# Kernel optimization log

Measured on AMD Instinct MI355X. Metric: run time of the kernel, lower is better.

Reference implementation:

```python
import jax, jax.numpy as jnp
import numpy as np

K = 16  # kNN neighbors (global k in the original source)
# channel progression of the 6 DynamicEdgeConv layers
DIMS = [3, 32, 128, 256, 64, 32, 16]


def _knn_idx(x, k):
    # x: [B, N, D] -> indices of k nearest neighbors (incl. self), [B, N, k]
    sq = jnp.sum(x * x, axis=-1)                                   # [B, N]
    d = sq[:, :, None] + sq[:, None, :] - 2.0 * jnp.einsum('bnd,bmd->bnm', x, x)
    _, idx = jax.lax.top_k(-d, k)                                  # smallest distances
    return idx


def _edge_conv(x, W1, b1, W2, b2, k):
    # DynamicEdgeConv with mean aggregation: message = MLP([x_i, x_j - x_i])
    idx = _knn_idx(x, k)                                           # [B, N, k]
    xj = jax.vmap(lambda xb, ib: xb[ib])(x, idx)                   # [B, N, k, D]
    xi = jnp.broadcast_to(x[:, :, None, :], xj.shape)
    e = jnp.concatenate([xi, xj - xi], axis=-1)                    # [B, N, k, 2D]
    h = jax.nn.relu(e @ W1 + b1)
    h = jax.nn.relu(h @ W2 + b2)
    return jnp.mean(h, axis=2)                                     # [B, N, d_out]


def setup_inputs() -> dict:
    key = jax.random.key(0)
    ks = jax.random.split(key, 32)
    inp = {'x': jax.random.normal(ks[0], (8, 2048, 3), dtype=jnp.float32)}
    for l in range(6):
        din, dout = DIMS[l], DIMS[l + 1]
        s1 = 1.0 / np.sqrt(2 * din)
        s2 = 1.0 / np.sqrt(2 * dout)
        inp[f'W1_{l}'] = jax.random.normal(ks[1 + 4 * l], (2 * din, 2 * dout), dtype=jnp.float32) * s1
        inp[f'b1_{l}'] = jnp.zeros((2 * dout,), dtype=jnp.float32)
        inp[f'W2_{l}'] = jax.random.normal(ks[2 + 4 * l], (2 * dout, dout), dtype=jnp.float32) * s2
        inp[f'b2_{l}'] = jnp.zeros((dout,), dtype=jnp.float32)
    inp['Wf'] = jax.random.normal(ks[30], (16, 2), dtype=jnp.float32) * 0.25
    inp['bf'] = jnp.zeros((2,), dtype=jnp.float32)
    return inp


def reference(x, W1_0, b1_0, W2_0, b2_0, W1_1, b1_1, W2_1, b2_1,
              W1_2, b1_2, W2_2, b2_2, W1_3, b1_3, W2_3, b2_3,
              W1_4, b1_4, W2_4, b2_4, W1_5, b1_5, W2_5, b2_5, Wf, bf):
    params = [(W1_0, b1_0, W2_0, b2_0), (W1_1, b1_1, W2_1, b2_1),
              (W1_2, b1_2, W2_2, b2_2), (W1_3, b1_3, W2_3, b2_3),
              (W1_4, b1_4, W2_4, b2_4), (W1_5, b1_5, W2_5, b2_5)]
    for (W1, b1, W2, b2) in params:
        x = _edge_conv(x, W1, b1, W2, b2, K)
        x = jax.nn.relu(x)  # extra ReLU from forward (dropout is eval-mode identity)
    pooled = jnp.mean(x, axis=1)        # global_mean_pool over nodes -> [B, 16]
    return pooled @ Wf + bf             # [B, 2]
```

## Files before the change

### kernel.cpp

```cpp
#include <hip/hip_runtime.h>
#include <math.h>

#define NPTS 2048
#define NB 8
#define BN 16384
#define KNN 16

typedef _Float16 half4 __attribute__((ext_vector_type(4)));
typedef _Float16 half8 __attribute__((ext_vector_type(8)));
typedef float floatx16 __attribute__((ext_vector_type(16)));

__global__ __launch_bounds__(256) void sqprep_kernel(const float* __restrict__ X,
                                                     float* __restrict__ SQ,
                                                     const float* __restrict__ W1,
                                                     const float* __restrict__ b1,
                                                     float* __restrict__ Wcat,
                                                     float* __restrict__ bcat,
                                                     int din, int d2,
                                                     const float* __restrict__ W2,
                                                     _Float16* __restrict__ W2H,
                                                     _Float16* __restrict__ W2L,
                                                     int dout, int pb) {
    const int bid = blockIdx.x;
    if (bid < BN / 256) {
        int g = bid * 256 + threadIdx.x;
        const float* row = X + (size_t)g * din;
        float s = 0.f;
        for (int d = 0; d < din; ++d) s = fmaf(row[d], row[d], s);
        SQ[g] = s;
    } else if (bid < BN / 256 + pb) {
        int n4 = 2 * d2;
        int total = din * n4;
        int i = (bid - BN / 256) * 256 + threadIdx.x;
        if (i < total) {
            int d = i / n4, c = i - d * n4;
            float v;
            if (c < d2) v = W1[d * d2 + c] - W1[(din + d) * d2 + c];
            else        v = W1[(din + d) * d2 + (c - d2)];
            Wcat[i] = v;
        }
        if (i < n4) bcat[i] = (i < d2) ? b1[i] : 0.f;
    } else {
        int i = (bid - BN / 256 - pb) * 256 + threadIdx.x;
        if (i < d2 * dout) {
            int k = i / dout, c = i - k * dout;
            float wv = W2[i];
            _Float16 hv = (_Float16)wv;
            float rv = wv - (float)hv;
            W2H[(size_t)c * d2 + k] = hv;
            W2L[(size_t)c * d2 + k] = (_Float16)rv;
        }
    }
}

template <int DIN>
__global__ __launch_bounds__(256) void gram_kernel(const float* __restrict__ X,
                                                   const float* __restrict__ SQ,
                                                   float* __restrict__ DT) {
    __shared__ float As[32][132];
    __shared__ float Bs[32][132];
    const int t = threadIdx.x;
    const int tx = t & 15, ty = t >> 4;
    int bid = blockIdx.x;
    int bi = 0;
    while (bid >= 16 - bi) { bid -= 16 - bi; ++bi; }
    const int bj = bi + bid;
    const int i0 = bi * 128;
    const int j0 = bj * 128;
    const int z = blockIdx.z;
    const float* Xb = X + (size_t)z * NPTS * DIN;
    const float* SQb = SQ + (size_t)z * NPTS;
    float* DTb = DT + (size_t)z * NPTS * NPTS;

    const int e = t & 127;

    float acc[8][8];
    #pragma unroll
    for (int i = 0; i < 8; ++i)
        #pragma unroll
        for (int j = 0; j < 8; ++j) acc[i][j] = 0.f;

    if constexpr (DIN % 32 == 0) {
        const int rh = (t >> 7) * 16;
        const float* Ar = Xb + (size_t)(i0 + e) * DIN;
        const float* Br = Xb + (size_t)(j0 + e) * DIN;
        for (int k0 = 0; k0 < DIN; k0 += 32) {
            #pragma unroll
            for (int h = 0; h < 4; ++h) {
                float4 a = *(const float4*)(Ar + k0 + rh + h * 4);
                float4 b = *(const float4*)(Br + k0 + rh + h * 4);
                As[rh + h * 4 + 0][e] = a.x; As[rh + h * 4 + 1][e] = a.y;
                As[rh + h * 4 + 2][e] = a.z; As[rh + h * 4 + 3][e] = a.w;
                Bs[rh + h * 4 + 0][e] = b.x; Bs[rh + h * 4 + 1][e] = b.y;
                Bs[rh + h * 4 + 2][e] = b.z; Bs[rh + h * 4 + 3][e] = b.w;
            }
            __syncthreads();
            #pragma unroll
            for (int r = 0; r < 32; ++r) {
                float4 a0 = *(const float4*)&As[r][ty * 4];
                float4 a1 = *(const float4*)&As[r][64 + ty * 4];
                float4 b0 = *(const float4*)&Bs[r][tx * 4];
                float4 b1 = *(const float4*)&Bs[r][64 + tx * 4];
                float av[8] = {a0.x, a0.y, a0.z, a0.w, a1.x, a1.y, a1.z, a1.w};
                float bv[8] = {b0.x, b0.y, b0.z, b0.w, b1.x, b1.y, b1.z, b1.w};
                #pragma unroll
                for (int i = 0; i < 8; ++i)
                    #pragma unroll
                    for (int j = 0; j < 8; ++j)
                        acc[i][j] = fmaf(av[i], bv[j], acc[i][j]);
            }
            __syncthreads();
        }
    } else {
        const int rh = (t >> 7) * 8;
        #pragma unroll
        for (int i = 0; i < 8; ++i) {
            int k = rh + i;
            As[rh + i][e] = (k < DIN) ? Xb[(size_t)(i0 + e) * DIN + k] : 0.f;
            Bs[rh + i][e] = (k < DIN) ? Xb[(size_t)(j0 + e) * DIN + k] : 0.f;
        }
        __syncthreads();
        #pragma unroll
        for (int r = 0; r < 16; ++r) {
            float4 a0 = *(const float4*)&As[r][ty * 4];
            float4 a1 = *(const float4*)&As[r][64 + ty * 4];
            float4 b0 = *(const float4*)&Bs[r][tx * 4];
            float4 b1 = *(const float4*)&Bs[r][64 + tx * 4];
            float av[8] = {a0.x, a0.y, a0.z, a0.w, a1.x, a1.y, a1.z, a1.w};
            float bv[8] = {b0.x, b0.y, b0.z, b0.w, b1.x, b1.y, b1.z, b1.w};
            #pragma unroll
            for (int i = 0; i < 8; ++i)
                #pragma unroll
                for (int j = 0; j < 8; ++j)
                    acc[i][j] = fmaf(av[i], bv[j], acc[i][j]);
        }
        __syncthreads();
    }

    float sqi[8], sqj[8];
    #pragma unroll
    for (int i = 0; i < 8; ++i) {
        int ro = (i < 4) ? (ty * 4 + i) : (64 + ty * 4 + (i - 4));
        sqi[i] = SQb[i0 + ro];
    }
    #pragma unroll
    for (int j = 0; j < 8; ++j) {
        int co = (j < 4) ? (tx * 4 + j) : (64 + tx * 4 + (j - 4));
        sqj[j] = SQb[j0 + co];
    }
    #pragma unroll
    for (int i = 0; i < 8; ++i) {
        int ro = (i < 4) ? (ty * 4 + i) : (64 + ty * 4 + (i - 4));
        float* out = DTb + (size_t)(i0 + ro) * NPTS + j0;
        float4 o0, o1;
        o0.x = (sqi[i] + sqj[0]) - 2.f * acc[i][0];
        o0.y = (sqi[i] + sqj[1]) - 2.f * acc[i][1];
        o0.z = (sqi[i] + sqj[2]) - 2.f * acc[i][2];
        o0.w = (sqi[i] + sqj[3]) - 2.f * acc[i][3];
        o1.x = (sqi[i] + sqj[4]) - 2.f * acc[i][4];
        o1.y = (sqi[i] + sqj[5]) - 2.f * acc[i][5];
        o1.z = (sqi[i] + sqj[6]) - 2.f * acc[i][6];
        o1.w = (sqi[i] + sqj[7]) - 2.f * acc[i][7];
        *(float4*)(out + tx * 4) = o0;
        *(float4*)(out + 64 + tx * 4) = o1;
    }
    if (bi != bj) {
        #pragma unroll
        for (int j = 0; j < 8; ++j) {
            int co = (j < 4) ? (tx * 4 + j) : (64 + tx * 4 + (j - 4));
            float* out = DTb + (size_t)(j0 + co) * NPTS + i0;
            float4 o0, o1;
            o0.x = (sqi[0] + sqj[j]) - 2.f * acc[0][j];
            o0.y = (sqi[1] + sqj[j]) - 2.f * acc[1][j];
            o0.z = (sqi[2] + sqj[j]) - 2.f * acc[2][j];
            o0.w = (sqi[3] + sqj[j]) - 2.f * acc[3][j];
            o1.x = (sqi[4] + sqj[j]) - 2.f * acc[4][j];
            o1.y = (sqi[5] + sqj[j]) - 2.f * acc[5][j];
            o1.z = (sqi[6] + sqj[j]) - 2.f * acc[6][j];
            o1.w = (sqi[7] + sqj[j]) - 2.f * acc[7][j];
            *(float4*)(out + ty * 4) = o0;
            *(float4*)(out + 64 + ty * 4) = o1;
        }
    }
}

__global__ __launch_bounds__(256) void knn_select_kernel(const float* __restrict__ DT,
                                                         int* __restrict__ IDX, int qoff) {
    const int t = threadIdx.x;
    const int w = t >> 6, lane = t & 63;
    const int q = blockIdx.x * 4 + w;
    const float* dq = DT + (size_t)q * NPTS;
    const int l4 = lane << 2;

    float vals[32];
    #pragma unroll
    for (int s = 0; s < 8; ++s) {
        float4 v = *(const float4*)(dq + s * 256 + l4);
        vals[s * 4 + 0] = v.x; vals[s * 4 + 1] = v.y;
        vals[s * 4 + 2] = v.z; vals[s * 4 + 3] = v.w;
    }
    unsigned rm = 0;
    float best = INFINITY; int bslot = 32;
    #pragma unroll
    for (int sl = 0; sl < 32; ++sl)
        if (vals[sl] < best) { best = vals[sl]; bslot = sl; }

    for (int rep = 0; rep < KNN; ++rep) {
        int bj = (bslot < 32) ? ((bslot >> 2) * 256 + l4 + (bslot & 3)) : NPTS;
        float gb = best; int gj = bj;
        #pragma unroll
        for (int off = 1; off < 64; off <<= 1) {
            float ov = __shfl_xor(gb, off);
            int oj = __shfl_xor(gj, off);
            if (ov < gb || (ov == gb && oj < gj)) { gb = ov; gj = oj; }
        }
        if (lane == 0) IDX[(size_t)(qoff + q) * KNN + rep] = gj;
        if (((gj >> 2) & 63) == lane) {
            int slot = ((gj >> 8) << 2) | (gj & 3);
            rm |= (1u << slot);
            best = INFINITY; bslot = 32;
            #pragma unroll
            for (int sl = 0; sl < 32; ++sl)
                if (!(rm & (1u << sl)) && vals[sl] < best) { best = vals[sl]; bslot = sl; }
        }
    }
}

template <int KK, int NN>
__global__ __launch_bounds__(256) void gemm_big_kernel(const float* __restrict__ A,
                                                       const float* __restrict__ B,
                                                       const float* __restrict__ bias,
                                                       float* __restrict__ C) {
    __shared__ float As[32][132];
    __shared__ float Bs[32][132];
    const int t = threadIdx.x;
    const int tx = t & 15, ty = t >> 4;
    const int m0 = blockIdx.x * 128;
    const int c0 = blockIdx.y * 128;

    float acc[8][8];
    #pragma unroll
    for (int i = 0; i < 8; ++i)
        #pragma unroll
        for (int j = 0; j < 8; ++j) acc[i][j] = 0.f;

    const int e = t & 127;
    const int rh = (t >> 7) * 16;
    const float* Ar = A + (size_t)(m0 + e) * KK + rh;
    const int br = t & 31;
    const int bc = (t >> 5) * 16;
    const float* Wbase = B + (size_t)br * NN + c0 + bc;

    for (int k0 = 0; k0 < KK; k0 += 32) {
        #pragma unroll
        for (int h = 0; h < 4; ++h) {
            float4 a = *(const float4*)(Ar + k0 + h * 4);
            As[rh + h * 4 + 0][e] = a.x; As[rh + h * 4 + 1][e] = a.y;
            As[rh + h * 4 + 2][e] = a.z; As[rh + h * 4 + 3][e] = a.w;
            *(float4*)&Bs[br][bc + h * 4] = *(const float4*)(Wbase + (size_t)k0 * NN + h * 4);
        }
        __syncthreads();
        #pragma unroll
        for (int r = 0; r < 32; ++r) {
            float4 a0 = *(const float4*)&As[r][ty * 4];
            float4 a1 = *(const float4*)&As[r][64 + ty * 4];
            float4 b0 = *(const float4*)&Bs[r][tx * 4];
            float4 b1 = *(const float4*)&Bs[r][64 + tx * 4];
            float av[8] = {a0.x, a0.y, a0.z, a0.w, a1.x, a1.y, a1.z, a1.w};
            float bv[8] = {b0.x, b0.y, b0.z, b0.w, b1.x, b1.y, b1.z, b1.w};
            #pragma unroll
            for (int i = 0; i < 8; ++i)
                #pragma unroll
                for (int j = 0; j < 8; ++j)
                    acc[i][j] = fmaf(av[i], bv[j], acc[i][j]);
        }
        __syncthreads();
    }

    float bvv[8];
    #pragma unroll
    for (int j = 0; j < 8; ++j) {
        int co = (j < 4) ? (tx * 4 + j) : (64 + tx * 4 + (j - 4));
        bvv[j] = bias[c0 + co];
    }
    #pragma unroll
    for (int i = 0; i < 8; ++i) {
        int ro = (i < 4) ? (ty * 4 + i) : (64 + ty * 4 + (i - 4));
        float* out = C + (size_t)(m0 + ro) * NN + c0;
        float4 o0, o1;
        o0.x = acc[i][0] + bvv[0]; o0.y = acc[i][1] + bvv[1];
        o0.z = acc[i][2] + bvv[2]; o0.w = acc[i][3] + bvv[3];
        o1.x = acc[i][4] + bvv[4]; o1.y = acc[i][5] + bvv[5];
        o1.z = acc[i][6] + bvv[6]; o1.w = acc[i][7] + bvv[7];
        *(float4*)(out + tx * 4) = o0;
        *(float4*)(out + 64 + tx * 4) = o1;
    }
}

template <int KK, int NN>
__global__ __launch_bounds__(256) void gemm_pq_kernel(const float* __restrict__ A,
                                                      const float* __restrict__ B,
                                                      const float* __restrict__ bias,
                                                      float* __restrict__ C) {
    __shared__ float As[16][68];
    __shared__ float Bs[16][64];
    const int t = threadIdx.x;
    const int tx = t & 15, ty = t >> 4;
    const int m0 = blockIdx.x * 64;
    const int c0 = blockIdx.y * 64;
    float acc[4][4];
    #pragma unroll
    for (int i = 0; i < 4; ++i)
        #pragma unroll
        for (int j = 0; j < 4; ++j) acc[i][j] = 0.f;

    constexpr int KCH = (KK + 15) / 16;
    for (int kc = 0; kc < KCH; ++kc) {
        const int k0 = kc * 16;
        {
            int m = t & 63;
            int r4 = (t >> 6) * 4;
            if constexpr (KK % 16 == 0) {
                float4 v = *(const float4*)(A + (size_t)(m0 + m) * KK + k0 + r4);
                As[r4 + 0][m] = v.x; As[r4 + 1][m] = v.y;
                As[r4 + 2][m] = v.z; As[r4 + 3][m] = v.w;
            } else {
                #pragma unroll
                for (int i = 0; i < 4; ++i) {
                    int r = r4 + i;
                    As[r][m] = (k0 + r < KK) ? A[(size_t)(m0 + m) * KK + k0 + r] : 0.f;
                }
            }
        }
        {
            int r = t >> 4;
            int c = (t & 15) * 4;
            float4 v = make_float4(0.f, 0.f, 0.f, 0.f);
            if (k0 + r < KK) v = *(const float4*)(B + (size_t)(k0 + r) * NN + c0 + c);
            *(float4*)&Bs[r][c] = v;
        }
        __syncthreads();
        #pragma unroll
        for (int r = 0; r < 16; ++r) {
            float4 a4 = *(const float4*)&As[r][ty * 4];
            float4 b4 = *(const float4*)&Bs[r][tx * 4];
            float av[4] = {a4.x, a4.y, a4.z, a4.w};
            float bv[4] = {b4.x, b4.y, b4.z, b4.w};
            #pragma unroll
            for (int i = 0; i < 4; ++i)
                #pragma unroll
                for (int j = 0; j < 4; ++j)
                    acc[i][j] = fmaf(av[i], bv[j], acc[i][j]);
        }
        __syncthreads();
    }
    float4 bv4 = *(const float4*)(bias + c0 + tx * 4);
    float bv[4] = {bv4.x, bv4.y, bv4.z, bv4.w};
    #pragma unroll
    for (int i = 0; i < 4; ++i) {
        float4 o;
        o.x = acc[i][0] + bv[0];
        o.y = acc[i][1] + bv[1];
        o.z = acc[i][2] + bv[2];
        o.w = acc[i][3] + bv[3];
        *(float4*)(C + (size_t)(m0 + ty * 4 + i) * NN + c0 + tx * 4) = o;
    }
}

template <int D2, int DOUT>
__global__ __launch_bounds__(256) void edge_kernel(const float* __restrict__ PQ,
                                                   const int* __restrict__ IDX,
                                                   const float* __restrict__ W2,
                                                   const float* __restrict__ b2,
                                                   float* __restrict__ Xn) {
    constexpr int N4 = 2 * D2;
    __shared__ float As[16][68];
    __shared__ float Bs[16][64];
    __shared__ int gjs[64];
    const int t = threadIdx.x;
    const int tx = t & 15, ty = t >> 4;
    const int nb = blockIdx.x * 4;
    const int c0 = blockIdx.y * 64;

    if (t < 64) {
        int node = nb + (t >> 4);
        int bstart = (node / NPTS) * NPTS;
        gjs[t] = bstart + IDX[(size_t)node * KNN + (t & 15)];
    }
    __syncthreads();

    float acc[4][4];
    #pragma unroll
    for (int i = 0; i < 4; ++i)
        #pragma unroll
        for (int j = 0; j < 4; ++j) acc[i][j] = 0.f;

    const int e = t & 63;
    const int r4 = (t >> 6) * 4;
    const int gi = nb + (e >> 4);

    for (int k0 = 0; k0 < D2; k0 += 16) {
        {
            int gj = gjs[e];
            float4 p = *(const float4*)(PQ + (size_t)gi * N4 + k0 + r4);
            float4 q = *(const float4*)(PQ + (size_t)gj * N4 + D2 + k0 + r4);
            As[r4 + 0][e] = fmaxf(p.x + q.x, 0.f);
            As[r4 + 1][e] = fmaxf(p.y + q.y, 0.f);
            As[r4 + 2][e] = fmaxf(p.z + q.z, 0.f);
            As[r4 + 3][e] = fmaxf(p.w + q.w, 0.f);
        }
        {
            int r = t >> 4;
            int c = (t & 15) * 4;
            float4 v = make_float4(0.f, 0.f, 0.f, 0.f);
            if (c0 + c < DOUT) v = *(const float4*)(W2 + (size_t)(k0 + r) * DOUT + c0 + c);
            *(float4*)&Bs[r][c] = v;
        }
        __syncthreads();
        #pragma unroll
        for (int r = 0; r < 16; ++r) {
            float4 a4 = *(const float4*)&As[r][ty * 4];
            float4 b4 = *(const float4*)&Bs[r][tx * 4];
            float av[4] = {a4.x, a4.y, a4.z, a4.w};
            float bv[4] = {b4.x, b4.y, b4.z, b4.w};
            #pragma unroll
            for (int i = 0; i < 4; ++i)
                #pragma unroll
                for (int j = 0; j < 4; ++j)
                    acc[i][j] = fmaf(av[i], bv[j], acc[i][j]);
        }
        __syncthreads();
    }

    float bv[4];
    #pragma unroll
    for (int j = 0; j < 4; ++j) {
        int c = c0 + tx * 4 + j;
        bv[j] = (c < DOUT) ? b2[c] : 0.f;
    }
    float s[4];
    #pragma unroll
    for (int j = 0; j < 4; ++j) {
        float ss = 0.f;
        #pragma unroll
        for (int i = 0; i < 4; ++i) ss += fmaxf(acc[i][j] + bv[j], 0.f);
        s[j] = ss;
    }
    #pragma unroll
    for (int j = 0; j < 4; ++j) Bs[ty][tx * 4 + j] = s[j];
    __syncthreads();
    if ((ty & 3) == 0) {
        int node = nb + (ty >> 2);
        #pragma unroll
        for (int j = 0; j < 4; ++j) {
            int c = c0 + tx * 4 + j;
            if (c < DOUT) {
                int cc = tx * 4 + j;
                float tot = Bs[ty][cc] + Bs[ty + 1][cc] + Bs[ty + 2][cc] + Bs[ty + 3][cc];
                Xn[(size_t)node * DOUT + c] = tot * (1.f / 16.f);
            }
        }
    }
}

template <int D2, int DOUT>
__global__ __launch_bounds__(256) void edge_big_mfma_kernel(const float* __restrict__ PQ,
                                                            const int* __restrict__ IDX,
                                                            const _Float16* __restrict__ W2H,
                                                            const _Float16* __restrict__ W2L,
                                                            const float* __restrict__ b2,
                                                            float* __restrict__ Xn) {
    constexpr int N4 = 2 * D2;
    __shared__ _Float16 Ah[128][40];
    __shared__ _Float16 Al[128][40];
    __shared__ _Float16 Bh[128][40];
    __shared__ _Float16 Bl[128][40];
    __shared__ int gjs[128];
    const int t = threadIdx.x;
    const int nb8 = blockIdx.x * 8;
    const int c0 = blockIdx.y * 128;

    if (t < 128) {
        int node = nb8 + (t >> 4);
        int bstart = (node / NPTS) * NPTS;
        gjs[t] = bstart + IDX[(size_t)node * KNN + (t & 15)];
    }
    __syncthreads();

    const int e = t & 127;
    const int rh = (t >> 7) * 16;
    const int gi = nb8 + (e >> 4);
    const int gj = gjs[e];
    const float* Prow = PQ + (size_t)gi * N4;
    const float* Qrow = PQ + (size_t)gj * N4 + D2;
    const _Float16* WHrow = W2H + (size_t)(c0 + e) * D2;
    const _Float16* WLrow = W2L + (size_t)(c0 + e) * D2;

    const int w = t >> 6;
    const int lane = t & 63;
    const int wr = (w >> 1) * 64;
    const int wc = (w & 1) * 64;
    const int lr = lane & 31;
    const int lk = (lane >> 5) * 8;
    const int hsel = lane >> 5;

    floatx16 acc[2][2];
    #pragma unroll
    for (int i = 0; i < 2; ++i)
        #pragma unroll
        for (int j = 0; j < 2; ++j)
            #pragma unroll
            for (int r = 0; r < 16; ++r) acc[i][j][r] = 0.f;

    float4 pp[4], qq[4];
    #pragma unroll
    for (int h = 0; h < 4; ++h) {
        pp[h] = *(const float4*)(Prow + rh + h * 4);
        qq[h] = *(const float4*)(Qrow + rh + h * 4);
    }

    for (int k0 = 0; k0 < D2; k0 += 32) {
        half8 wh0 = *(const half8*)(WHrow + k0 + rh);
        half8 wh1 = *(const half8*)(WHrow + k0 + rh + 8);
        half8 wl0 = *(const half8*)(WLrow + k0 + rh);
        half8 wl1 = *(const half8*)(WLrow + k0 + rh + 8);
        #pragma unroll
        for (int h = 0; h < 4; ++h) {
            float a0 = fmaxf(pp[h].x + qq[h].x, 0.f);
            float a1 = fmaxf(pp[h].y + qq[h].y, 0.f);
            float a2 = fmaxf(pp[h].z + qq[h].z, 0.f);
            float a3 = fmaxf(pp[h].w + qq[h].w, 0.f);
            _Float16 h0 = (_Float16)a0, h1 = (_Float16)a1, h2 = (_Float16)a2, h3 = (_Float16)a3;
            half4 hv, lv;
            hv.x = h0; hv.y = h1; hv.z = h2; hv.w = h3;
            lv.x = (_Float16)(a0 - (float)h0);
            lv.y = (_Float16)(a1 - (float)h1);
            lv.z = (_Float16)(a2 - (float)h2);
            lv.w = (_Float16)(a3 - (float)h3);
            *(half4*)&Ah[e][rh + h * 4] = hv;
            *(half4*)&Al[e][rh + h * 4] = lv;
        }
        *(half8*)&Bh[e][rh]     = wh0;
        *(half8*)&Bh[e][rh + 8] = wh1;
        *(half8*)&Bl[e][rh]     = wl0;
        *(half8*)&Bl[e][rh + 8] = wl1;
        __syncthreads();
        if (k0 + 32 < D2) {
            #pragma unroll
            for (int h = 0; h < 4; ++h) {
                pp[h] = *(const float4*)(Prow + k0 + 32 + rh + h * 4);
                qq[h] = *(const float4*)(Qrow + k0 + 32 + rh + h * 4);
            }
        }
        #pragma unroll
        for (int ks = 0; ks < 2; ++ks) {
            const int kb = ks * 16 + lk;
            half8 bf0  = *(const half8*)&Bh[wc + lr][kb];
            half8 blf0 = *(const half8*)&Bl[wc + lr][kb];
            half8 bf1  = *(const half8*)&Bh[wc + 32 + lr][kb];
            half8 blf1 = *(const half8*)&Bl[wc + 32 + lr][kb];
            #pragma unroll
            for (int i = 0; i < 2; ++i) {
                half8 af  = *(const half8*)&Ah[wr + i * 32 + lr][kb];
                half8 alf = *(const half8*)&Al[wr + i * 32 + lr][kb];
                acc[i][0] = __builtin_amdgcn_mfma_f32_32x32x16_f16(af,  bf0,  acc[i][0], 0, 0, 0);
                acc[i][0] = __builtin_amdgcn_mfma_f32_32x32x16_f16(af,  blf0, acc[i][0], 0, 0, 0);
                acc[i][0] = __builtin_amdgcn_mfma_f32_32x32x16_f16(alf, bf0,  acc[i][0], 0, 0, 0);
                acc[i][1] = __builtin_amdgcn_mfma_f32_32x32x16_f16(af,  bf1,  acc[i][1], 0, 0, 0);
                acc[i][1] = __builtin_amdgcn_mfma_f32_32x32x16_f16(af,  blf1, acc[i][1], 0, 0, 0);
                acc[i][1] = __builtin_amdgcn_mfma_f32_32x32x16_f16(alf, bf1,  acc[i][1], 0, 0, 0);
            }
        }
        asm volatile("" ::: "memory");
        __builtin_amdgcn_s_barrier();
        asm volatile("" ::: "memory");
    }

    float bb[2];
    bb[0] = b2[c0 + wc + lr];
    bb[1] = b2[c0 + wc + 32 + lr];
    #pragma unroll
    for (int i = 0; i < 2; ++i) {
        int node0 = nb8 + ((wr + i * 32) >> 4);
        #pragma unroll
        for (int j = 0; j < 2; ++j) {
            float sA = 0.f, sB = 0.f;
            #pragma unroll
            for (int r = 0; r < 8; ++r)  sA += fmaxf(acc[i][j][r] + bb[j], 0.f);
            #pragma unroll
            for (int r = 8; r < 16; ++r) sB += fmaxf(acc[i][j][r] + bb[j], 0.f);
            sA += __shfl_xor(sA, 32);
            sB += __shfl_xor(sB, 32);
            if (hsel == 0) {
                int col = c0 + wc + j * 32 + lr;
                Xn[(size_t)node0 * DOUT + col] = sA * (1.f / 16.f);
                Xn[(size_t)(node0 + 1) * DOUT + col] = sB * (1.f / 16.f);
            }
        }
    }
}

template <int D2, int DOUT>
__global__ __launch_bounds__(256) void edge_mid_mfma_kernel(const float* __restrict__ PQ,
                                                            const int* __restrict__ IDX,
                                                            const _Float16* __restrict__ W2H,
                                                            const _Float16* __restrict__ W2L,
                                                            const float* __restrict__ b2,
                                                            float* __restrict__ Xn) {
    constexpr int N4 = 2 * D2;
    __shared__ _Float16 Ah[128][40];
    __shared__ _Float16 Al[128][40];
    __shared__ _Float16 Bh[64][40];
    __shared__ _Float16 Bl[64][40];
    __shared__ int gjs[128];
    const int t = threadIdx.x;
    const int nb8 = blockIdx.x * 8;

    if (t < 128) {
        int node = nb8 + (t >> 4);
        int bstart = (node / NPTS) * NPTS;
        gjs[t] = bstart + IDX[(size_t)node * KNN + (t & 15)];
    }
    __syncthreads();

    const int e = t & 127;
    const int rh = (t >> 7) * 16;
    const int gi = nb8 + (e >> 4);
    const int gj = gjs[e];
    const float* Prow = PQ + (size_t)gi * N4;
    const float* Qrow = PQ + (size_t)gj * N4 + D2;
    const int wrB = t & 63;
    const int wkB = (t >> 6) * 8;
    const _Float16* WHrow = W2H + (size_t)wrB * D2 + wkB;
    const _Float16* WLrow = W2L + (size_t)wrB * D2 + wkB;

    const int w = t >> 6;
    const int lane = t & 63;
    const int wr = (w >> 1) * 64;
    const int wc = (w & 1) * 32;
    const int lr = lane & 31;
    const int lk = (lane >> 5) * 8;
    const int hsel = lane >> 5;

    floatx16 acc[2];
    #pragma unroll
    for (int i = 0; i < 2; ++i)
        #pragma unroll
        for (int r = 0; r < 16; ++r) acc[i][r] = 0.f;

    float4 pp[4], qq[4];
    #pragma unroll
    for (int h = 0; h < 4; ++h) {
        pp[h] = *(const float4*)(Prow + rh + h * 4);
        qq[h] = *(const float4*)(Qrow + rh + h * 4);
    }

    for (int k0 = 0; k0 < D2; k0 += 32) {
        half8 wh0 = *(const half8*)(WHrow + k0);
        half8 wl0 = *(const half8*)(WLrow + k0);
        #pragma unroll
        for (int h = 0; h < 4; ++h) {
            float a0 = fmaxf(pp[h].x + qq[h].x, 0.f);
            float a1 = fmaxf(pp[h].y + qq[h].y, 0.f);
            float a2 = fmaxf(pp[h].z + qq[h].z, 0.f);
            float a3 = fmaxf(pp[h].w + qq[h].w, 0.f);
            _Float16 h0 = (_Float16)a0, h1 = (_Float16)a1, h2 = (_Float16)a2, h3 = (_Float16)a3;
            half4 hv, lv;
            hv.x = h0; hv.y = h1; hv.z = h2; hv.w = h3;
            lv.x = (_Float16)(a0 - (float)h0);
            lv.y = (_Float16)(a1 - (float)h1);
            lv.z = (_Float16)(a2 - (float)h2);
            lv.w = (_Float16)(a3 - (float)h3);
            *(half4*)&Ah[e][rh + h * 4] = hv;
            *(half4*)&Al[e][rh + h * 4] = lv;
        }
        *(half8*)&Bh[wrB][wkB] = wh0;
        *(half8*)&Bl[wrB][wkB] = wl0;
        __syncthreads();
        if (k0 + 32 < D2) {
            #pragma unroll
            for (int h = 0; h < 4; ++h) {
                pp[h] = *(const float4*)(Prow + k0 + 32 + rh + h * 4);
                qq[h] = *(const float4*)(Qrow + k0 + 32 + rh + h * 4);
            }
        }
        #pragma unroll
        for (int ks = 0; ks < 2; ++ks) {
            const int kb = ks * 16 + lk;
            half8 bf0  = *(const half8*)&Bh[wc + lr][kb];
            half8 blf0 = *(const half8*)&Bl[wc + lr][kb];
            #pragma unroll
            for (int i = 0; i < 2; ++i) {
                half8 af  = *(const half8*)&Ah[wr + i * 32 + lr][kb];
                half8 alf = *(const half8*)&Al[wr + i * 32 + lr][kb];
                acc[i] = __builtin_amdgcn_mfma_f32_32x32x16_f16(af,  bf0,  acc[i], 0, 0, 0);
                acc[i] = __builtin_amdgcn_mfma_f32_32x32x16_f16(af,  blf0, acc[i], 0, 0, 0);
                acc[i] = __builtin_amdgcn_mfma_f32_32x32x16_f16(alf, bf0,  acc[i], 0, 0, 0);
            }
        }
        asm volatile("" ::: "memory");
        __builtin_amdgcn_s_barrier();
        asm volatile("" ::: "memory");
    }

    float bb = b2[wc + lr];
    #pragma unroll
    for (int i = 0; i < 2; ++i) {
        int node0 = nb8 + ((wr + i * 32) >> 4);
        float sA = 0.f, sB = 0.f;
        #pragma unroll
        for (int r = 0; r < 8; ++r)  sA += fmaxf(acc[i][r] + bb, 0.f);
        #pragma unroll
        for (int r = 8; r < 16; ++r) sB += fmaxf(acc[i][r] + bb, 0.f);
        sA += __shfl_xor(sA, 32);
        sB += __shfl_xor(sB, 32);
        if (hsel == 0) {
            int col = wc + lr;
            Xn[(size_t)node0 * DOUT + col] = sA * (1.f / 16.f);
            Xn[(size_t)(node0 + 1) * DOUT + col] = sB * (1.f / 16.f);
        }
    }
}

__global__ __launch_bounds__(256) void final_kernel(const float* __restrict__ X,
                                                    const float* __restrict__ Wf,
                                                    const float* __restrict__ bfin,
                                                    float* __restrict__ out) {
    __shared__ float red[16][17];
    __shared__ float pool[16];
    const int b = blockIdx.x;
    const int t = threadIdx.x;
    const int c = t & 15, rg = t >> 4;
    float s = 0.f;
    for (int n = rg; n < NPTS; n += 16) s += X[(size_t)(b * NPTS + n) * 16 + c];
    red[rg][c] = s;
    __syncthreads();
    if (t < 16) {
        float tot = 0.f;
        #pragma unroll
        for (int i = 0; i < 16; ++i) tot += red[i][t];
        pool[t] = tot * (1.f / NPTS);
    }
    __syncthreads();
    if (t < 2) {
        float a = bfin[t];
        #pragma unroll
        for (int cc = 0; cc < 16; ++cc) a = fmaf(pool[cc], Wf[cc * 2 + t], a);
        out[b * 2 + t] = a;
    }
}

template <int DIN, int DOUT>
static void run_layer(const float* Xin, float* Xout, float* PQ, float* SQ, int* IDX,
                      float* WCAT, float* BCAT, _Float16* W2H, _Float16* W2L,
                      const float* W1, const float* b1, const float* W2, const float* b2,
                      hipStream_t stream) {
    constexpr int D2 = 2 * DOUT;
    constexpr int N4 = 2 * D2;
    constexpr int prep_blocks = (DIN * N4 + 255) / 256;
    constexpr int w2_blocks = (DOUT >= 64) ? ((D2 * DOUT + 255) / 256) : 0;
    sqprep_kernel<<<BN / 256 + prep_blocks + w2_blocks, 256, 0, stream>>>(
        Xin, SQ, W1, b1, WCAT, BCAT, DIN, D2, W2, W2H, W2L,
        (DOUT >= 64) ? DOUT : 0, prep_blocks);
    for (int h = 0; h < 2; ++h) {
        dim3 gg(136, 1, 4);
        gram_kernel<DIN><<<gg, 256, 0, stream>>>(Xin + (size_t)h * 4 * NPTS * DIN,
                                                 SQ + (size_t)h * 4 * NPTS, PQ);
        knn_select_kernel<<<2048, 256, 0, stream>>>(PQ, IDX, h * 8192);
    }
    if constexpr (N4 % 128 == 0 && DIN % 32 == 0) {
        dim3 g1(BN / 128, N4 / 128);
        gemm_big_kernel<DIN, N4><<<g1, 256, 0, stream>>>(Xin, WCAT, BCAT, PQ);
    } else {
        dim3 g1(BN / 64, N4 / 64);
        gemm_pq_kernel<DIN, N4><<<g1, 256, 0, stream>>>(Xin, WCAT, BCAT, PQ);
    }
    if constexpr (DOUT >= 128) {
        dim3 g2(BN / 8, DOUT / 128);
        edge_big_mfma_kernel<D2, DOUT><<<g2, 256, 0, stream>>>(PQ, IDX, W2H, W2L, b2, Xout);
    } else if constexpr (DOUT == 64) {
        dim3 g2(BN / 8, 1);
        edge_mid_mfma_kernel<D2, DOUT><<<g2, 256, 0, stream>>>(PQ, IDX, W2H, W2L, b2, Xout);
    } else {
        dim3 g2(BN / 4, (DOUT + 63) / 64);
        edge_kernel<D2, DOUT><<<g2, 256, 0, stream>>>(PQ, IDX, W2, b2, Xout);
    }
}

extern "C" void kernel_launch(void* const* d_in, const int* in_sizes, int n_in,
                              void* d_out, int out_size, void* d_ws, size_t ws_size,
                              hipStream_t stream) {
    (void)in_sizes; (void)n_in; (void)out_size; (void)ws_size;
    const float* x = (const float*)d_in[0];
    const float* W1a[6]; const float* b1a[6]; const float* W2a[6]; const float* b2a[6];
    for (int l = 0; l < 6; ++l) {
        W1a[l] = (const float*)d_in[1 + 4 * l];
        b1a[l] = (const float*)d_in[2 + 4 * l];
        W2a[l] = (const float*)d_in[3 + 4 * l];
        b2a[l] = (const float*)d_in[4 + 4 * l];
    }
    const float* Wf = (const float*)d_in[25];
    const float* bfin = (const float*)d_in[26];

    float* ws = (float*)d_ws;
    float* X0   = ws;
    float* X1   = X0 + (size_t)BN * 256;
    float* PQ   = X1 + (size_t)BN * 256;
    float* SQ   = PQ + (size_t)BN * 1024;
    int*   IDX  = (int*)(SQ + BN);
    float* WCAT = (float*)(IDX + (size_t)BN * KNN);
    float* BCAT = WCAT + 131072;
    _Float16* W2H = (_Float16*)(BCAT + 1024);
    _Float16* W2L = W2H + 131072;

    run_layer<3,   32>(x,  X0, PQ, SQ, IDX, WCAT, BCAT, W2H, W2L, W1a[0], b1a[0], W2a[0], b2a[0], stream);
    run_layer<32, 128>(X0, X1, PQ, SQ, IDX, WCAT, BCAT, W2H, W2L, W1a[1], b1a[1], W2a[1], b2a[1], stream);
    run_layer<128,256>(X1, X0, PQ, SQ, IDX, WCAT, BCAT, W2H, W2L, W1a[2], b1a[2], W2a[2], b2a[2], stream);
    run_layer<256, 64>(X0, X1, PQ, SQ, IDX, WCAT, BCAT, W2H, W2L, W1a[3], b1a[3], W2a[3], b2a[3], stream);
    run_layer<64,  32>(X1, X0, PQ, SQ, IDX, WCAT, BCAT, W2H, W2L, W1a[4], b1a[4], W2a[4], b2a[4], stream);
    run_layer<32,  16>(X0, X1, PQ, SQ, IDX, WCAT, BCAT, W2H, W2L, W1a[5], b1a[5], W2a[5], b2a[5], stream);
    final_kernel<<<NB, 256, 0, stream>>>(X1, Wf, bfin, (float*)d_out);
}
```

Measured before the change: 1.852 ms.

## Load W2 MFMA B-fragments directly from global into registers, skipping LDS

In the big and mid edge MFMA kernels, the W2 hi/lo weight fragments are now read straight from global memory into registers in MFMA operand layout, instead of being staged through shared memory. The next tile's fragments are prefetched during the current tile's MFMAs. The Q and P loads are split around the compute so memory latency overlaps with math, and the __syncthreads is replaced by an explicit lgkmcnt wait plus barrier. This cuts LDS traffic and footprint, which may raise occupancy, but adds register pressure and uncoalesced global weight reads that rely on cache reuse across blocks.

```diff
diff --git a/kernel.cpp b/kernel.cpp
--- a/kernel.cpp
+++ b/kernel.cpp
@@ -463,6 +463,8 @@
     }
 }
 
+struct BFragBig { half8 h0, l0, h1, l1, h2, l2, h3, l3; };
+
 template <int D2, int DOUT>
 __global__ __launch_bounds__(256) void edge_big_mfma_kernel(const float* __restrict__ PQ,
                                                             const int* __restrict__ IDX,
@@ -473,8 +475,6 @@
     constexpr int N4 = 2 * D2;
     __shared__ _Float16 Ah[128][40];
     __shared__ _Float16 Al[128][40];
-    __shared__ _Float16 Bh[128][40];
-    __shared__ _Float16 Bl[128][40];
     __shared__ int gjs[128];
     const int t = threadIdx.x;
     const int nb8 = blockIdx.x * 8;
@@ -493,8 +493,6 @@
     const int gj = gjs[e];
     const float* Prow = PQ + (size_t)gi * N4;
     const float* Qrow = PQ + (size_t)gj * N4 + D2;
-    const _Float16* WHrow = W2H + (size_t)(c0 + e) * D2;
-    const _Float16* WLrow = W2L + (size_t)(c0 + e) * D2;
 
     const int w = t >> 6;
     const int lane = t & 63;
@@ -504,6 +502,11 @@
     const int lk = (lane >> 5) * 8;
     const int hsel = lane >> 5;
 
+    const _Float16* WH0 = W2H + (size_t)(c0 + wc + lr) * D2;
+    const _Float16* WH1 = WH0 + (size_t)32 * D2;
+    const _Float16* WL0 = W2L + (size_t)(c0 + wc + lr) * D2;
+    const _Float16* WL1 = WL0 + (size_t)32 * D2;
+
     floatx16 acc[2][2];
     #pragma unroll
     for (int i = 0; i < 2; ++i)
@@ -513,17 +516,23 @@
             for (int r = 0; r < 16; ++r) acc[i][j][r] = 0.f;
 
     float4 pp[4], qq[4];
+    BFragBig bb;
     #pragma unroll
     for (int h = 0; h < 4; ++h) {
         pp[h] = *(const float4*)(Prow + rh + h * 4);
         qq[h] = *(const float4*)(Qrow + rh + h * 4);
     }
+    bb.h0 = *(const half8*)(WH0 + lk);
+    bb.l0 = *(const half8*)(WL0 + lk);
+    bb.h1 = *(const half8*)(WH1 + lk);
+    bb.l1 = *(const half8*)(WL1 + lk);
+    bb.h2 = *(const half8*)(WH0 + 16 + lk);
+    bb.l2 = *(const half8*)(WL0 + 16 + lk);
+    bb.h3 = *(const half8*)(WH1 + 16 + lk);
+    bb.l3 = *(const half8*)(WL1 + 16 + lk);
 
     for (int k0 = 0; k0 < D2; k0 += 32) {
-        half8 wh0 = *(const half8*)(WHrow + k0 + rh);
-        half8 wh1 = *(const half8*)(WHrow + k0 + rh + 8);
-        half8 wl0 = *(const half8*)(WLrow + k0 + rh);
-        half8 wl1 = *(const half8*)(WLrow + k0 + rh + 8);
+        const bool nxt = (k0 + 32 < D2);
         #pragma unroll
         for (int h = 0; h < 4; ++h) {
             float a0 = fmaxf(pp[h].x + qq[h].x, 0.f);
@@ -540,45 +549,57 @@
             *(half4*)&Ah[e][rh + h * 4] = hv;
             *(half4*)&Al[e][rh + h * 4] = lv;
         }
-        *(half8*)&Bh[e][rh]     = wh0;
-        *(half8*)&Bh[e][rh + 8] = wh1;
-        *(half8*)&Bl[e][rh]     = wl0;
-        *(half8*)&Bl[e][rh + 8] = wl1;
-        __syncthreads();
-        if (k0 + 32 < D2) {
-            #pragma unroll
-            for (int h = 0; h < 4; ++h) {
+        if (nxt) {
+            #pragma unroll
+            for (int h = 0; h < 4; ++h)
+                qq[h] = *(const float4*)(Qrow + k0 + 32 + rh + h * 4);
+        }
+        asm volatile("s_waitcnt lgkmcnt(0)" ::: "memory");
+        __builtin_amdgcn_s_barrier();
+        asm volatile("" ::: "memory");
+        #pragma unroll
+        for (int i = 0; i < 2; ++i) {
+            half8 af  = *(const half8*)&Ah[wr + i * 32 + lr][lk];
+            half8 alf = *(const half8*)&Al[wr + i * 32 + lr][lk];
+            acc[i][0] = __builtin_amdgcn_mfma_f32_32x32x16_f16(af,  bb.h0, acc[i][0], 0, 0, 0);
+            acc[i][0] = __builtin_amdgcn_mfma_f32_32x32x16_f16(af,  bb.l0, acc[i][0], 0, 0, 0);
+            acc[i][0] = __builtin_amdgcn_mfma_f32_32x32x16_f16(alf, bb.h0, acc[i][0], 0, 0, 0);
+            acc[i][1] = __builtin_amdgcn_mfma_f32_32x32x16_f16(af,  bb.h1, acc[i][1], 0, 0, 0);
+            acc[i][1] = __builtin_amdgcn_mfma_f32_32x32x16_f16(af,  bb.l1, acc[i][1], 0, 0, 0);
+            acc[i][1] = __builtin_amdgcn_mfma_f32_32x32x16_f16(alf, bb.h1, acc[i][1], 0, 0, 0);
+        }
+        #pragma unroll
+        for (int i = 0; i < 2; ++i) {
+            half8 af  = *(const half8*)&Ah[wr + i * 32 + lr][16 + lk];
+            half8 alf = *(const half8*)&Al[wr + i * 32 + lr][16 + lk];
+            acc[i][0] = __builtin_amdgcn_mfma_f32_32x32x16_f16(af,  bb.h2, acc[i][0], 0, 0, 0);
+            acc[i][0] = __builtin_amdgcn_mfma_f32_32x32x16_f16(af,  bb.l2, acc[i][0], 0, 0, 0);
+            acc[i][0] = __builtin_amdgcn_mfma_f32_32x32x16_f16(alf, bb.h2, acc[i][0], 0, 0, 0);
+            acc[i][1] = __builtin_amdgcn_mfma_f32_32x32x16_f16(af,  bb.h3, acc[i][1], 0, 0, 0);
+            acc[i][1] = __builtin_amdgcn_mfma_f32_32x32x16_f16(af,  bb.l3, acc[i][1], 0, 0, 0);
+            acc[i][1] = __builtin_amdgcn_mfma_f32_32x32x16_f16(alf, bb.h3, acc[i][1], 0, 0, 0);
+        }
+        if (nxt) {
+            #pragma unroll
+            for (int h = 0; h < 4; ++h)
                 pp[h] = *(const float4*)(Prow + k0 + 32 + rh + h * 4);
-                qq[h] = *(const float4*)(Qrow + k0 + 32 + rh + h * 4);
-            }
-        }
-        #pragma unroll
-        for (int ks = 0; ks < 2; ++ks) {
-            const int kb = ks * 16 + lk;
-            half8 bf0  = *(const half8*)&Bh[wc + lr][kb];
-            half8 blf0 = *(const half8*)&Bl[wc + lr][kb];
-            half8 bf1  = *(const half8*)&Bh[wc + 32 + lr][kb];
-            half8 blf1 = *(const half8*)&Bl[wc + 32 + lr][kb];
-            #pragma unroll
-            for (int i = 0; i < 2; ++i) {
-                half8 af  = *(const half8*)&Ah[wr + i * 32 + lr][kb];
-                half8 alf = *(const half8*)&Al[wr + i * 32 + lr][kb];
-                acc[i][0] = __builtin_amdgcn_mfma_f32_32x32x16_f16(af,  bf0,  acc[i][0], 0, 0, 0);
-                acc[i][0] = __builtin_amdgcn_mfma_f32_32x32x16_f16(af,  blf0, acc[i][0], 0, 0, 0);
-                acc[i][0] = __builtin_amdgcn_mfma_f32_32x32x16_f16(alf, bf0,  acc[i][0], 0, 0, 0);
-                acc[i][1] = __builtin_amdgcn_mfma_f32_32x32x16_f16(af,  bf1,  acc[i][1], 0, 0, 0);
-                acc[i][1] = __builtin_amdgcn_mfma_f32_32x32x16_f16(af,  blf1, acc[i][1], 0, 0, 0);
-                acc[i][1] = __builtin_amdgcn_mfma_f32_32x32x16_f16(alf, bf1,  acc[i][1], 0, 0, 0);
-            }
+            bb.h0 = *(const half8*)(WH0 + k0 + 32 + lk);
+            bb.l0 = *(const half8*)(WL0 + k0 + 32 + lk);
+            bb.h1 = *(const half8*)(WH1 + k0 + 32 + lk);
+            bb.l1 = *(const half8*)(WL1 + k0 + 32 + lk);
+            bb.h2 = *(const half8*)(WH0 + k0 + 48 + lk);
+            bb.l2 = *(const half8*)(WL0 + k0 + 48 + lk);
+            bb.h3 = *(const half8*)(WH1 + k0 + 48 + lk);
+            bb.l3 = *(const half8*)(WL1 + k0 + 48 + lk);
         }
         asm volatile("" ::: "memory");
         __builtin_amdgcn_s_barrier();
         asm volatile("" ::: "memory");
     }
 
-    float bb[2];
-    bb[0] = b2[c0 + wc + lr];
-    bb[1] = b2[c0 + wc + 32 + lr];
+    float bbias[2];
+    bbias[0] = b2[c0 + wc + lr];
+    bbias[1] = b2[c0 + wc + 32 + lr];
     #pragma unroll
     for (int i = 0; i < 2; ++i) {
         int node0 = nb8 + ((wr + i * 32) >> 4);
@@ -586,9 +607,9 @@
         for (int j = 0; j < 2; ++j) {
             float sA = 0.f, sB = 0.f;
             #pragma unroll
-            for (int r = 0; r < 8; ++r)  sA += fmaxf(acc[i][j][r] + bb[j], 0.f);
-            #pragma unroll
-            for (int r = 8; r < 16; ++r) sB += fmaxf(acc[i][j][r] + bb[j], 0.f);
+            for (int r = 0; r < 8; ++r)  sA += fmaxf(acc[i][j][r] + bbias[j], 0.f);
+            #pragma unroll
+            for (int r = 8; r < 16; ++r) sB += fmaxf(acc[i][j][r] + bbias[j], 0.f);
             sA += __shfl_xor(sA, 32);
             sB += __shfl_xor(sB, 32);
             if (hsel == 0) {
@@ -599,6 +620,8 @@
         }
     }
 }
+
+struct BFragMid { half8 h0, l0, h1, l1; };
 
 template <int D2, int DOUT>
 __global__ __launch_bounds__(256) void edge_mid_mfma_kernel(const float* __restrict__ PQ,
@@ -610,8 +633,6 @@
     constexpr int N4 = 2 * D2;
     __shared__ _Float16 Ah[128][40];
     __shared__ _Float16 Al[128][40];
-    __shared__ _Float16 Bh[64][40];
-    __shared__ _Float16 Bl[64][40];
     __shared__ int gjs[128];
     const int t = threadIdx.x;
     const int nb8 = blockIdx.x * 8;
@@ -629,10 +650,6 @@
     const int gj = gjs[e];
     const float* Prow = PQ + (size_t)gi * N4;
     const float* Qrow = PQ + (size_t)gj * N4 + D2;
-    const int wrB = t & 63;
-    const int wkB = (t >> 6) * 8;
-    const _Float16* WHrow = W2H + (size_t)wrB * D2 + wkB;
-    const _Float16* WLrow = W2L + (size_t)wrB * D2 + wkB;
 
     const int w = t >> 6;
     const int lane = t & 63;
@@ -642,6 +659,9 @@
     const int lk = (lane >> 5) * 8;
     const int hsel = lane >> 5;
 
+    const _Float16* WH0 = W2H + (size_t)(wc + lr) * D2;
+    const _Float16* WL0 = W2L + (size_t)(wc + lr) * D2;
+
     floatx16 acc[2];
     #pragma unroll
     for (int i = 0; i < 2; ++i)
@@ -649,15 +669,19 @@
         for (int r = 0; r < 16; ++r) acc[i][r] = 0.f;
 
     float4 pp[4], qq[4];
+    BFragMid bb;
     #pragma unroll
     for (int h = 0; h < 4; ++h) {
         pp[h] = *(const float4*)(Prow + rh + h * 4);
         qq[h] = *(const float4*)(Qrow + rh + h * 4);
     }
+    bb.h0 = *(const half8*)(WH0 + lk);
+    bb.l0 = *(const half8*)(WL0 + lk);
+    bb.h1 = *(const half8*)(WH0 + 16 + lk);
+    bb.l1 = *(const half8*)(WL0 + 16 + lk);
 
     for (int k0 = 0; k0 < D2; k0 += 32) {
-        half8 wh0 = *(const half8*)(WHrow + k0);
-        half8 wl0 = *(const half8*)(WLrow + k0);
+        const bool nxt = (k0 + 32 < D2);
         #pragma unroll
         for (int h = 0; h < 4; ++h) {
             float a0 = fmaxf(pp[h].x + qq[h].x, 0.f);
@@ -674,44 +698,53 @@
             *(half4*)&Ah[e][rh + h * 4] = hv;
             *(half4*)&Al[e][rh + h * 4] = lv;
         }
-        *(half8*)&Bh[wrB][wkB] = wh0;
-        *(half8*)&Bl[wrB][wkB] = wl0;
-        __syncthreads();
-        if (k0 + 32 < D2) {
-            #pragma unroll
-            for (int h = 0; h < 4; ++h) {
+        if (nxt) {
+            #pragma unroll
+            for (int h = 0; h < 4; ++h)
+                qq[h] = *(const float4*)(Qrow + k0 + 32 + rh + h * 4);
+        }
+        asm volatile("s_waitcnt lgkmcnt(0)" ::: "memory");
+        __builtin_amdgcn_s_barrier();
+        asm volatile("" ::: "memory");
+        #pragma unroll
+        for (int i = 0; i < 2; ++i) {
+            half8 af  = *(const half8*)&Ah[wr + i * 32 + lr][lk];
+            half8 alf = *(const half8*)&Al[wr + i * 32 + lr][lk];
+            acc[i] = __builtin_amdgcn_mfma_f32_32x32x16_f16(af,  bb.h0, acc[i], 0, 0, 0);
+            acc[i] = __builtin_amdgcn_mfma_f32_32x32x16_f16(af,  bb.l0, acc[i], 0, 0, 0);
+            acc[i] = __builtin_amdgcn_mfma_f32_32x32x16_f16(alf, bb.h0, acc[i], 0, 0, 0);
+        }
+        #pragma unroll
+        for (int i = 0; i < 2; ++i) {
+            half8 af  = *(const half8*)&Ah[wr + i * 32 + lr][16 + lk];
+            half8 alf = *(const half8*)&Al[wr + i * 32 + lr][16 + lk];
+            acc[i] = __builtin_amdgcn_mfma_f32_32x32x16_f16(af,  bb.h1, acc[i], 0, 0, 0);
+            acc[i] = __builtin_amdgcn_mfma_f32_32x32x16_f16(af,  bb.l1, acc[i], 0, 0, 0);
+            acc[i] = __builtin_amdgcn_mfma_f32_32x32x16_f16(alf, bb.h1, acc[i], 0, 0, 0);
+        }
+        if (nxt) {
+            #pragma unroll
+            for (int h = 0; h < 4; ++h)
                 pp[h] = *(const float4*)(Prow + k0 + 32 + rh + h * 4);
-                qq[h] = *(const float4*)(Qrow + k0 + 32 + rh + h * 4);
-            }
-        }
-        #pragma unroll
-        for (int ks = 0; ks < 2; ++ks) {
-            const int kb = ks * 16 + lk;
-            half8 bf0  = *(const half8*)&Bh[wc + lr][kb];
-            half8 blf0 = *(const half8*)&Bl[wc + lr][kb];
-            #pragma unroll
-            for (int i = 0; i < 2; ++i) {
-                half8 af  = *(const half8*)&Ah[wr + i * 32 + lr][kb];
-                half8 alf = *(const half8*)&Al[wr + i * 32 + lr][kb];
-                acc[i] = __builtin_amdgcn_mfma_f32_32x32x16_f16(af,  bf0,  acc[i], 0, 0, 0);
-                acc[i] = __builtin_amdgcn_mfma_f32_32x32x16_f16(af,  blf0, acc[i], 0, 0, 0);
-                acc[i] = __builtin_amdgcn_mfma_f32_32x32x16_f16(alf, bf0,  acc[i], 0, 0, 0);
-            }
+            bb.h0 = *(const half8*)(WH0 + k0 + 32 + lk);
+            bb.l0 = *(const half8*)(WL0 + k0 + 32 + lk);
+            bb.h1 = *(const half8*)(WH0 + k0 + 48 + lk);
+            bb.l1 = *(const half8*)(WL0 + k0 + 48 + lk);
         }
         asm volatile("" ::: "memory");
         __builtin_amdgcn_s_barrier();
         asm volatile("" ::: "memory");
     }
 
-    float bb = b2[wc + lr];
+    float bbias = b2[wc + lr];
     #pragma unroll
     for (int i = 0; i < 2; ++i) {
         int node0 = nb8 + ((wr + i * 32) >> 4);
         float sA = 0.f, sB = 0.f;
         #pragma unroll
-        for (int r = 0; r < 8; ++r)  sA += fmaxf(acc[i][r] + bb, 0.f);
-        #pragma unroll
-        for (int r = 8; r < 16; ++r) sB += fmaxf(acc[i][r] + bb, 0.f);
+        for (int r = 0; r < 8; ++r)  sA += fmaxf(acc[i][r] + bbias, 0.f);
+        #pragma unroll
+        for (int r = 8; r < 16; ++r) sB += fmaxf(acc[i][r] + bbias, 0.f);
         sA += __shfl_xor(sA, 32);
         sB += __shfl_xor(sB, 32);
         if (hsel == 0) {
```

Measured after the change: 1.959 ms. 5.8% more time.
